# Kernel optimization log

Measured on AMD Instinct MI355X. Metric: run time of the kernel, lower is better.

The kernel has to match this reference:

```python
import jax, jax.numpy as jnp
import numpy as np

B, H, W, D = 64, 56, 56, 128
WS = 7            # window size per axis
NH = 4            # attention heads
L = 2             # transformer layers (layer 1 is shifted)
HID = 4 * D
G1, G2 = H // WS, W // WS
G, N = G1 * G2, WS * WS
SH = WS // 2      # cyclic shift


def _build_attn_mask():
    # faithful port of ShiftWindow mask construction (numpy constants)
    img = np.zeros((H, W), dtype=np.float32)
    sl = (slice(0, -WS), slice(-WS, -SH), slice(-SH, None))
    idx = 0
    for s0 in sl:
        for s1 in sl:
            img[s0, s1] = idx
            idx += 1
    win = img.reshape(G1, WS, G2, WS).transpose(0, 2, 1, 3).reshape(G, N)
    diff = win[:, None, :] - win[:, :, None]          # [G, N, N]
    return jnp.asarray(np.where(diff != 0, -100.0, 0.0).astype(np.float32))

ATTN_MASK = _build_attn_mask()


def setup_inputs() -> dict:
    key = jax.random.key(0)
    ks = jax.random.split(key, 8)
    s = 0.02
    return {
        'x': jax.random.normal(ks[0], (B, H, W, D), jnp.float32),
        'ln1_g': jnp.ones((L, D)), 'ln1_b': jnp.zeros((L, D)),
        'qkv_w': s * jax.random.normal(ks[1], (L, D, 3 * D)), 'qkv_b': jnp.zeros((L, 3 * D)),
        'proj_w': s * jax.random.normal(ks[2], (L, D, D)), 'proj_b': jnp.zeros((L, D)),
        'ln2_g': jnp.ones((L, D)), 'ln2_b': jnp.zeros((L, D)),
        'mlp_w1': s * jax.random.normal(ks[3], (L, D, HID)), 'mlp_b1': jnp.zeros((L, HID)),
        'mlp_w2': s * jax.random.normal(ks[4], (L, HID, D)), 'mlp_b2': jnp.zeros((L, D)),
        'ds_norm_g': jnp.ones((4 * D,)), 'ds_norm_b': jnp.zeros((4 * D,)),
        'ds_w': s * jax.random.normal(ks[5], (4 * D, 2 * D)),
    }


def _ln(x, g, b, eps=1e-5):
    m = jnp.mean(x, -1, keepdims=True)
    v = jnp.mean((x - m) ** 2, -1, keepdims=True)
    return (x - m) * jax.lax.rsqrt(v + eps) * g + b


def _partition(x):
    # [B, H, W, D] -> [B, G, N, D]
    x = x.reshape(B, G1, WS, G2, WS, D).transpose(0, 1, 3, 2, 4, 5)
    return x.reshape(B, G, N, D)


def _unpartition(xw):
    x = xw.reshape(B, G1, G2, WS, WS, D).transpose(0, 1, 3, 2, 4, 5)
    return x.reshape(B, H, W, D)


def _block(xw, mask, i, p):
    # pre-norm window attention
    h = _ln(xw, p['ln1_g'][i], p['ln1_b'][i])
    qkv = h @ p['qkv_w'][i] + p['qkv_b'][i]                 # [B,G,N,3D]
    q, k, v = jnp.split(qkv, 3, axis=-1)
    hd = D // NH
    q = q.reshape(B, G, N, NH, hd)
    k = k.reshape(B, G, N, NH, hd)
    v = v.reshape(B, G, N, NH, hd)
    scores = jnp.einsum('bgnhd,bgmhd->bghnm', q, k) / jnp.sqrt(jnp.float32(hd))
    if mask is not None:
        scores = scores + mask[None, :, None, :, :]         # [1,G,1,N,N]
    attn = jax.nn.softmax(scores, axis=-1)
    o = jnp.einsum('bghnm,bgmhd->bgnhd', attn, v).reshape(B, G, N, D)
    xw = xw + o @ p['proj_w'][i] + p['proj_b'][i]
    # MLP
    h = _ln(xw, p['ln2_g'][i], p['ln2_b'][i])
    h = jax.nn.gelu(h @ p['mlp_w1'][i] + p['mlp_b1'][i])
    return xw + h @ p['mlp_w2'][i] + p['mlp_b2'][i]


def reference(x, ln1_g, ln1_b, qkv_w, qkv_b, proj_w, proj_b, ln2_g, ln2_b,
              mlp_w1, mlp_b1, mlp_w2, mlp_b2, ds_norm_g, ds_norm_b, ds_w):
    p = dict(ln1_g=ln1_g, ln1_b=ln1_b, qkv_w=qkv_w, qkv_b=qkv_b,
             proj_w=proj_w, proj_b=proj_b, ln2_g=ln2_g, ln2_b=ln2_b,
             mlp_w1=mlp_w1, mlp_b1=mlp_b1, mlp_w2=mlp_w2, mlp_b2=mlp_b2)
    xw = _partition(x)
    for i in range(L):
        shift = (i % 2 == 1)
        if shift:
            xw = _partition(jnp.roll(_unpartition(xw), (-SH, -SH), axis=(1, 2)))
            xw = _block(xw, ATTN_MASK, i, p)
            xw = _partition(jnp.roll(_unpartition(xw), (SH, SH), axis=(1, 2)))
        else:
            xw = _block(xw, None, i, p)
    x = _unpartition(xw)
    # Downsample: 2x2 patch merge -> LN -> Linear(4D -> 2D) (no bias)
    x = x.reshape(B, H // 2, 2, W // 2, 2, D).transpose(0, 1, 3, 2, 4, 5)
    x = x.reshape(B, H // 2, W // 2, 4 * D)
    x = _ln(x, ds_norm_g, ds_norm_b) @ ds_w
    return x
```

## Files before the change

kernel.cpp:

```cpp
#include <hip/hip_runtime.h>
#include <hip/hip_bf16.h>


typedef short bf16x8 __attribute__((ext_vector_type(8)));
typedef float f32x4 __attribute__((ext_vector_type(4)));
typedef unsigned short u16;
typedef unsigned int u32;

#define MTOK 200704
#define DSTOK 50176

__device__ __forceinline__ u16 f2b(float f){
  u32 u = __float_as_uint(f);
  u += 0x7fffu + ((u >> 16) & 1u);
  return (u16)(u >> 16);
}
__device__ __forceinline__ float blo(u32 u){ return __uint_as_float(u << 16); }
__device__ __forceinline__ float bhi(u32 u){ return __uint_as_float(u & 0xffff0000u); }

__device__ __forceinline__ float gelu_tanh(float v){
  float u = 0.7978845608028654f * (v + 0.044715f * v * v * v);
  u = fminf(u, 10.f);
  float e = __expf(2.f * u);
  float t = (e - 1.f) / (e + 1.f);
  return 0.5f * v * (1.f + t);
}

__global__ void transpose_cvt(const float* __restrict__ src, u16* __restrict__ dst,
                              int K, int N){
  int e = blockIdx.x * 256 + threadIdx.x;
  if (e >= K * N) return;
  int k = e / N, n = e - k * N;
  dst[n * K + k] = f2b(src[e]);
}

template<int MODE>
__global__ __launch_bounds__(256) void ln_kernel(const float* __restrict__ src,
    const float* __restrict__ gw, const float* __restrict__ bw,
    u16* __restrict__ dst)
{
  int wv = threadIdx.x >> 6, lane = threadIdx.x & 63;
  int t = blockIdx.x * 4 + wv;
  long soff;
  if (MODE == 2) {
    soff = (long)t * 128;
  } else {
    int n = t % 49; int tq = t / 49; int gg = tq & 63; int b_ = tq >> 6;
    int r = n / 7, c = n - 7 * r;
    int h = (gg >> 3) * 7 + r, w = (gg & 7) * 7 + c;
    if (MODE == 1) { h += 3; if (h >= 56) h -= 56; w += 3; if (w >= 56) w -= 56; }
    soff = ((long)((b_ * 56 + h) * 56 + w)) * 128;
  }
  float2 v = *(const float2*)(src + soff + lane * 2);
  float s = v.x + v.y, s2 = v.x * v.x + v.y * v.y;
  #pragma unroll
  for (int o = 32; o; o >>= 1) { s += __shfl_xor(s, o); s2 += __shfl_xor(s2, o); }
  float mean = s * 0.0078125f;
  float var  = s2 * 0.0078125f - mean * mean;
  float rstd = rsqrtf(var + 1e-5f);
  int c0 = lane * 2;
  ushort2 o2;
  o2.x = f2b((v.x - mean) * rstd * gw[c0]   + bw[c0]);
  o2.y = f2b((v.y - mean) * rstd * gw[c0+1] + bw[c0+1]);
  *(ushort2*)(dst + (long)t * 128 + c0) = o2;
}

__global__ __launch_bounds__(256) void ds_ln_kernel(const float* __restrict__ x,
    const float* __restrict__ gw, const float* __restrict__ bw,
    u16* __restrict__ dst)
{
  int wv = threadIdx.x >> 6, lane = threadIdx.x & 63;
  int t = blockIdx.x * 4 + wv;
  int j = t % 28; int tq = t / 28; int i = tq % 28; int b_ = tq / 28;
  int e0 = lane * 8;
  int p = e0 >> 8, q = (e0 >> 7) & 1, d = e0 & 127;
  const float* src = x + ((long)((b_ * 56 + 2*i + p) * 56 + 2*j + q)) * 128 + d;
  float4 a  = *(const float4*)src;
  float4 b4 = *(const float4*)(src + 4);
  float vs[8] = {a.x, a.y, a.z, a.w, b4.x, b4.y, b4.z, b4.w};
  float s = 0.f, s2 = 0.f;
  #pragma unroll
  for (int u = 0; u < 8; u++) { s += vs[u]; s2 += vs[u] * vs[u]; }
  #pragma unroll
  for (int o = 32; o; o >>= 1) { s += __shfl_xor(s, o); s2 += __shfl_xor(s2, o); }
  float mean = s * (1.f / 512.f);
  float var  = s2 * (1.f / 512.f) - mean * mean;
  float rstd = rsqrtf(var + 1e-5f);
  u16 ov[8];
  #pragma unroll
  for (int u = 0; u < 8; u++) ov[u] = f2b((vs[u] - mean) * rstd * gw[e0+u] + bw[e0+u]);
  uint4 o4;
  o4.x = (u32)ov[0] | ((u32)ov[1] << 16);
  o4.y = (u32)ov[2] | ((u32)ov[3] << 16);
  o4.z = (u32)ov[4] | ((u32)ov[5] << 16);
  o4.w = (u32)ov[6] | ((u32)ov[7] << 16);
  *(uint4*)(dst + (long)t * 512 + e0) = o4;
}

template<int MASKED>
__global__ __launch_bounds__(256) void attn_mfma(const u16* __restrict__ qkv,
                                                 u16* __restrict__ obuf)
{
  __shared__ u16 Pls_all[4][64][72];
  const int h = threadIdx.x >> 6;
  const int lane = threadIdx.x & 63;
  const int c = lane & 15, g = lane >> 4;
  const int wi = blockIdx.x;
  const int g_ = wi & 63;
  const long t0 = (long)wi * 49;
  u16 (*Pls)[72] = Pls_all[h];

  bf16x8 qf[4], kf[4];
  #pragma unroll
  for (int mi = 0; mi < 4; mi++) {
    int r = 16*mi + c; r = r > 48 ? 48 : r;
    qf[mi] = *(const bf16x8*)(qkv + (t0 + r)*384 + h*32 + g*8);
  }
  #pragma unroll
  for (int ni = 0; ni < 4; ni++) {
    int r = 16*ni + c; r = r > 48 ? 48 : r;
    kf[ni] = *(const bf16x8*)(qkv + (t0 + r)*384 + 128 + h*32 + g*8);
  }

  f32x4 acc[4][4];
  const f32x4 zero4 = {0.f, 0.f, 0.f, 0.f};
  #pragma unroll
  for (int mi = 0; mi < 4; mi++)
    #pragma unroll
    for (int ni = 0; ni < 4; ni++)
      acc[mi][ni] = __builtin_amdgcn_mfma_f32_16x16x32_bf16(qf[mi], kf[ni], zero4, 0, 0, 0);

  bf16x8 vf[2][2];
  #pragma unroll
  for (int ni2 = 0; ni2 < 2; ni2++)
    #pragma unroll
    for (int ks = 0; ks < 2; ks++)
      #pragma unroll
      for (int jj = 0; jj < 8; jj++) {
        int k = ks*32 + 8*g + jj; k = k > 48 ? 48 : k;
        vf[ni2][ks][jj] = (short)qkv[(t0 + k)*384 + 256 + h*32 + 16*ni2 + c];
      }

  int rid_c[4];
  int g1b = 0, g2b = 0;
  if (MASKED) {
    g1b = (g_ >> 3) * 7; g2b = (g_ & 7) * 7;
    #pragma unroll
    for (int ni = 0; ni < 4; ni++) {
      int col = 16*ni + c; col = col > 48 ? 48 : col;
      int cr = col / 7, cc = col - 7*cr;
      int hh = g1b + cr, ww = g2b + cc;
      rid_c[ni] = (hh < 49 ? 0 : (hh < 53 ? 1 : 2)) * 3 + (ww < 49 ? 0 : (ww < 53 ? 1 : 2));
    }
  }

  #pragma unroll
  for (int mi = 0; mi < 4; mi++) {
    #pragma unroll
    for (int j = 0; j < 4; j++) {
      int rr = 16*mi + 4*g + j;
      int rid_r = 0;
      if (MASKED) {
        int r2 = rr > 48 ? 48 : rr;
        int rh = r2 / 7, rw = r2 - 7*rh;
        int hh = g1b + rh, ww = g2b + rw;
        rid_r = (hh < 49 ? 0 : (hh < 53 ? 1 : 2)) * 3 + (ww < 49 ? 0 : (ww < 53 ? 1 : 2));
      }
      float sv[4];
      #pragma unroll
      for (int ni = 0; ni < 4; ni++) {
        float s = acc[mi][ni][j] * 0.17677669529663687f;
        int col = 16*ni + c;
        if (col >= 49) s = -1e30f;
        else if (MASKED && rid_c[ni] != rid_r) s -= 100.f;
        sv[ni] = s;
      }
      float m4 = fmaxf(fmaxf(sv[0], sv[1]), fmaxf(sv[2], sv[3]));
      #pragma unroll
      for (int o = 1; o <= 8; o <<= 1) m4 = fmaxf(m4, __shfl_xor(m4, o));
      float p[4], sum = 0.f;
      #pragma unroll
      for (int ni = 0; ni < 4; ni++) { p[ni] = __expf(sv[ni] - m4); sum += p[ni]; }
      #pragma unroll
      for (int o = 1; o <= 8; o <<= 1) sum += __shfl_xor(sum, o);
      float rs = 1.f / sum;
      #pragma unroll
      for (int ni = 0; ni < 4; ni++)
        Pls[rr][16*ni + c] = f2b(p[ni] * rs);
    }
  }

  __syncthreads();

  f32x4 accO[4][2];
  #pragma unroll
  for (int mi = 0; mi < 4; mi++)
    #pragma unroll
    for (int ni2 = 0; ni2 < 2; ni2++) accO[mi][ni2] = zero4;
  #pragma unroll
  for (int mi = 0; mi < 4; mi++)
    #pragma unroll
    for (int ks = 0; ks < 2; ks++) {
      bf16x8 pa = *(const bf16x8*)(&Pls[16*mi + c][ks*32 + g*8]);
      #pragma unroll
      for (int ni2 = 0; ni2 < 2; ni2++)
        accO[mi][ni2] = __builtin_amdgcn_mfma_f32_16x16x32_bf16(pa, vf[ni2][ks], accO[mi][ni2], 0, 0, 0);
    }

  #pragma unroll
  for (int mi = 0; mi < 4; mi++)
    #pragma unroll
    for (int ni2 = 0; ni2 < 2; ni2++)
      #pragma unroll
      for (int j = 0; j < 4; j++) {
        int r = 16*mi + 4*g + j;
        if (r < 49)
          obuf[(t0 + r)*128 + h*32 + 16*ni2 + c] = f2b(accO[mi][ni2][j]);
      }
}

template<int K, int EPI>
__global__ __launch_bounds__(256) void gemm_kernel(
    const u16* __restrict__ A, const u16* __restrict__ Bt,
    const float* __restrict__ bias, int Ntot,
    u16* __restrict__ outb, float* __restrict__ outf,
    const float* __restrict__ resbase, int shift)
{
  __shared__ u16 As[128][72];
  __shared__ u16 Bs[128][72];
  const int tid = threadIdx.x;
  const int row0 = blockIdx.x * 128, col0 = blockIdx.y * 128;
  const int wv = tid >> 6, lane = tid & 63;
  const int m_off = (wv >> 1) * 64, n_off = (wv & 1) * 64;
  const int lr = lane & 15, lk = (lane >> 4) * 8;

  f32x4 acc[4][4];
  const f32x4 zero4 = {0.f, 0.f, 0.f, 0.f};
  #pragma unroll
  for (int a1 = 0; a1 < 4; a1++)
    #pragma unroll
    for (int a2 = 0; a2 < 4; a2++) acc[a1][a2] = zero4;

  for (int k0 = 0; k0 < K; k0 += 64) {
    __syncthreads();
    #pragma unroll
    for (int j = 0; j < 4; j++) {
      int ch = tid + 256 * j;
      int r = ch >> 3, cc = ch & 7;
      *(uint4*)(&As[r][cc*8]) = *(const uint4*)(A  + (long)(row0 + r) * K + k0 + cc*8);
      *(uint4*)(&Bs[r][cc*8]) = *(const uint4*)(Bt + (long)(col0 + r) * K + k0 + cc*8);
    }
    __syncthreads();
    #pragma unroll
    for (int kk = 0; kk < 64; kk += 32) {
      bf16x8 af[4], bfr[4];
      #pragma unroll
      for (int mi = 0; mi < 4; mi++)
        af[mi] = *(const bf16x8*)(&As[m_off + mi*16 + lr][kk + lk]);
      #pragma unroll
      for (int ni = 0; ni < 4; ni++)
        bfr[ni] = *(const bf16x8*)(&Bs[n_off + ni*16 + lr][kk + lk]);
      #pragma unroll
      for (int mi = 0; mi < 4; mi++)
        #pragma unroll
        for (int ni = 0; ni < 4; ni++)
          acc[mi][ni] = __builtin_amdgcn_mfma_f32_16x16x32_bf16(
              af[mi], bfr[ni], acc[mi][ni], 0, 0, 0);
    }
  }

  #pragma unroll
  for (int mi = 0; mi < 4; mi++) {
    #pragma unroll
    for (int j = 0; j < 4; j++) {
      int grow = row0 + m_off + mi*16 + (lane >> 4) * 4 + j;
      long obase = 0;
      if (EPI == 2) {
        int n = grow % 49; int tq = grow / 49; int gg = tq & 63; int b_ = tq >> 6;
        int r = n / 7, c = n - 7 * r;
        int hh = (gg >> 3) * 7 + r, ww = (gg & 7) * 7 + c;
        if (shift) { hh += 3; if (hh >= 56) hh -= 56; ww += 3; if (ww >= 56) ww -= 56; }
        obase = ((long)((b_ * 56 + hh) * 56 + ww)) * 128;
      }
      #pragma unroll
      for (int ni = 0; ni < 4; ni++) {
        int gcol = col0 + n_off + ni*16 + lr;
        float v = acc[mi][ni][j];
        if (EPI == 0) {
          v += bias[gcol];
          outb[(long)grow * Ntot + gcol] = f2b(v);
        } else if (EPI == 1) {
          v = gelu_tanh(v + bias[gcol]);
          outb[(long)grow * Ntot + gcol] = f2b(v);
        } else if (EPI == 2) {
          v += bias[gcol];
          outf[obase + gcol] = resbase[obase + gcol] + v;
        } else if (EPI == 3) {
          v += bias[gcol];
          outf[(long)grow * 128 + gcol] += v;
        } else {
          outf[(long)grow * Ntot + gcol] = v;
        }
      }
    }
  }
}

extern "C" void kernel_launch(void* const* d_in, const int* in_sizes, int n_in,
                              void* d_out, int out_size, void* d_ws, size_t ws_size,
                              hipStream_t stream)
{
  const float* x_in   = (const float*)d_in[0];
  const float* ln1_g  = (const float*)d_in[1];
  const float* ln1_b  = (const float*)d_in[2];
  const float* qkv_w  = (const float*)d_in[3];
  const float* qkv_b  = (const float*)d_in[4];
  const float* proj_w = (const float*)d_in[5];
  const float* proj_b = (const float*)d_in[6];
  const float* ln2_g  = (const float*)d_in[7];
  const float* ln2_b  = (const float*)d_in[8];
  const float* w1     = (const float*)d_in[9];
  const float* b1     = (const float*)d_in[10];
  const float* w2     = (const float*)d_in[11];
  const float* b2     = (const float*)d_in[12];
  const float* dsg    = (const float*)d_in[13];
  const float* dsb    = (const float*)d_in[14];
  const float* dsw    = (const float*)d_in[15];

  float* x_ws   = (float*)d_ws;
  u16* buf_h    = (u16*)(x_ws + (long)MTOK * 128);
  u16* buf_o    = buf_h;
  u16* buf_big  = buf_h + (long)MTOK * 128;
  u16* wts      = buf_big + (long)MTOK * 512;
  u16* qkv_wt   = wts;
  u16* proj_wt  = qkv_wt  + 2 * 49152;
  u16* w1t      = proj_wt + 2 * 16384;
  u16* w2t      = w1t     + 2 * 65536;
  u16* ds_wt    = w2t     + 2 * 65536;

  for (int i = 0; i < 2; i++) {
    transpose_cvt<<<(49152+255)/256, 256, 0, stream>>>(qkv_w  + i*49152, qkv_wt  + i*49152, 128, 384);
    transpose_cvt<<<(16384+255)/256, 256, 0, stream>>>(proj_w + i*16384, proj_wt + i*16384, 128, 128);
    transpose_cvt<<<(65536+255)/256, 256, 0, stream>>>(w1     + i*65536, w1t     + i*65536, 128, 512);
    transpose_cvt<<<(65536+255)/256, 256, 0, stream>>>(w2     + i*65536, w2t     + i*65536, 512, 128);
  }
  transpose_cvt<<<(131072+255)/256, 256, 0, stream>>>(dsw, ds_wt, 512, 256);

  for (int i = 0; i < 2; i++) {
    if (i == 0) ln_kernel<0><<<MTOK/4, 256, 0, stream>>>(x_in, ln1_g,       ln1_b,       buf_h);
    else        ln_kernel<1><<<MTOK/4, 256, 0, stream>>>(x_ws, ln1_g + 128, ln1_b + 128, buf_h);
    gemm_kernel<128,0><<<dim3(MTOK/128, 3), 256, 0, stream>>>(
        buf_h, qkv_wt + i*49152, qkv_b + i*384, 384, buf_big, nullptr, nullptr, 0);
    if (i == 0) attn_mfma<0><<<4096, 256, 0, stream>>>(buf_big, buf_o);
    else        attn_mfma<1><<<4096, 256, 0, stream>>>(buf_big, buf_o);
    gemm_kernel<128,2><<<dim3(MTOK/128, 1), 256, 0, stream>>>(
        buf_o, proj_wt + i*16384, proj_b + i*128, 128, nullptr, x_ws,
        (i == 0 ? x_in : (const float*)x_ws), i);
    ln_kernel<2><<<MTOK/4, 256, 0, stream>>>(x_ws, ln2_g + i*128, ln2_b + i*128, buf_h);
    gemm_kernel<128,1><<<dim3(MTOK/128, 4), 256, 0, stream>>>(
        buf_h, w1t + i*65536, b1 + i*512, 512, buf_big, nullptr, nullptr, 0);
    gemm_kernel<512,3><<<dim3(MTOK/128, 1), 256, 0, stream>>>(
        buf_big, w2t + i*65536, b2 + i*128, 128, nullptr, x_ws, x_ws, 0);
  }

  ds_ln_kernel<<<DSTOK/4, 256, 0, stream>>>(x_ws, dsg, dsb, buf_h);
  gemm_kernel<512,4><<<dim3(DSTOK/128, 2), 256, 0, stream>>>(
      buf_h, ds_wt, nullptr, 256, nullptr, (float*)d_out, nullptr, 0);
}
```

Before: 1.111 ms.

## Use direct global-to-LDS loads with XOR swizzle and LDS-staged vectorized epilogue

New measurement: 1.183 ms. 1.06x slower.

```diff
diff --git a/kernel.cpp b/kernel.cpp
--- a/kernel.cpp
+++ b/kernel.cpp
@@ -226,8 +226,11 @@
     u16* __restrict__ outb, float* __restrict__ outf,
     const float* __restrict__ resbase, int shift)
 {
-  __shared__ u16 As[128][72];
-  __shared__ u16 Bs[128][72];
+  __shared__ __align__(16) u16 sh[16384];
+  u16* Asl = sh;
+  u16* Bsl = sh + 8192;
+  float (*Cf)[128] = (float(*)[128])sh;
+
   const int tid = threadIdx.x;
   const int row0 = blockIdx.x * 128, col0 = blockIdx.y * 128;
   const int wv = tid >> 6, lane = tid & 63;
@@ -245,21 +248,30 @@
     __syncthreads();
     #pragma unroll
     for (int j = 0; j < 4; j++) {
-      int ch = tid + 256 * j;
+      int ch = tid + j * 256;
       int r = ch >> 3, cc = ch & 7;
-      *(uint4*)(&As[r][cc*8]) = *(const uint4*)(A  + (long)(row0 + r) * K + k0 + cc*8);
-      *(uint4*)(&Bs[r][cc*8]) = *(const uint4*)(Bt + (long)(col0 + r) * K + k0 + cc*8);
+      int col = k0 + ((cc * 8) ^ ((r & 7) << 3));
+      __builtin_amdgcn_global_load_lds(
+          (const __attribute__((address_space(1))) u32*)(A + (long)(row0 + r) * K + col),
+          (__attribute__((address_space(3))) u32*)(Asl + ch * 8), 16, 0, 0);
+      __builtin_amdgcn_global_load_lds(
+          (const __attribute__((address_space(1))) u32*)(Bt + (long)(col0 + r) * K + col),
+          (__attribute__((address_space(3))) u32*)(Bsl + ch * 8), 16, 0, 0);
     }
     __syncthreads();
     #pragma unroll
     for (int kk = 0; kk < 64; kk += 32) {
       bf16x8 af[4], bfr[4];
       #pragma unroll
-      for (int mi = 0; mi < 4; mi++)
-        af[mi] = *(const bf16x8*)(&As[m_off + mi*16 + lr][kk + lk]);
-      #pragma unroll
-      for (int ni = 0; ni < 4; ni++)
-        bfr[ni] = *(const bf16x8*)(&Bs[n_off + ni*16 + lr][kk + lk]);
+      for (int mi = 0; mi < 4; mi++) {
+        int R = m_off + mi*16 + lr;
+        af[mi] = *(const bf16x8*)&Asl[R*64 + ((kk + lk) ^ ((R & 7) << 3))];
+      }
+      #pragma unroll
+      for (int ni = 0; ni < 4; ni++) {
+        int R = n_off + ni*16 + lr;
+        bfr[ni] = *(const bf16x8*)&Bsl[R*64 + ((kk + lk) ^ ((R & 7) << 3))];
+      }
       #pragma unroll
       for (int mi = 0; mi < 4; mi++)
         #pragma unroll
@@ -269,38 +281,58 @@
     }
   }
 
-  #pragma unroll
-  for (int mi = 0; mi < 4; mi++) {
-    #pragma unroll
-    for (int j = 0; j < 4; j++) {
-      int grow = row0 + m_off + mi*16 + (lane >> 4) * 4 + j;
-      long obase = 0;
-      if (EPI == 2) {
+  const int g = lane >> 4;
+  #pragma unroll
+  for (int half = 0; half < 2; half++) {
+    __syncthreads();
+    if ((wv >> 1) == half) {
+      #pragma unroll
+      for (int mi = 0; mi < 4; mi++)
+        #pragma unroll
+        for (int ni = 0; ni < 4; ni++)
+          #pragma unroll
+          for (int j = 0; j < 4; j++) {
+            int lrow = mi*16 + 4*g + j;
+            int col  = n_off + ni*16 + lr;
+            Cf[lrow][col ^ ((lrow & 7) << 2)] = acc[mi][ni][j];
+          }
+    }
+    __syncthreads();
+    #pragma unroll
+    for (int jj = 0; jj < 8; jj++) {
+      int ch = tid + jj * 256;
+      int r = ch >> 5, c4 = ch & 31;
+      float4 v = *(const float4*)&Cf[r][(c4*4) ^ ((r & 7) << 2)];
+      int grow = row0 + half*64 + r;
+      int gcol = col0 + c4*4;
+      if (EPI == 0 || EPI == 1) {
+        float4 b4 = *(const float4*)&bias[gcol];
+        float v0 = v.x + b4.x, v1 = v.y + b4.y, v2 = v.z + b4.z, v3 = v.w + b4.w;
+        if (EPI == 1) { v0 = gelu_tanh(v0); v1 = gelu_tanh(v1); v2 = gelu_tanh(v2); v3 = gelu_tanh(v3); }
+        uint2 o2;
+        o2.x = (u32)f2b(v0) | ((u32)f2b(v1) << 16);
+        o2.y = (u32)f2b(v2) | ((u32)f2b(v3) << 16);
+        *(uint2*)(outb + (long)grow * Ntot + gcol) = o2;
+      } else if (EPI == 2) {
+        float4 b4 = *(const float4*)&bias[gcol];
         int n = grow % 49; int tq = grow / 49; int gg = tq & 63; int b_ = tq >> 6;
-        int r = n / 7, c = n - 7 * r;
-        int hh = (gg >> 3) * 7 + r, ww = (gg & 7) * 7 + c;
+        int rr = n / 7, cc = n - 7 * rr;
+        int hh = (gg >> 3) * 7 + rr, ww = (gg & 7) * 7 + cc;
         if (shift) { hh += 3; if (hh >= 56) hh -= 56; ww += 3; if (ww >= 56) ww -= 56; }
-        obase = ((long)((b_ * 56 + hh) * 56 + ww)) * 128;
-      }
-      #pragma unroll
-      for (int ni = 0; ni < 4; ni++) {
-        int gcol = col0 + n_off + ni*16 + lr;
-        float v = acc[mi][ni][j];
-        if (EPI == 0) {
-          v += bias[gcol];
-          outb[(long)grow * Ntot + gcol] = f2b(v);
-        } else if (EPI == 1) {
-          v = gelu_tanh(v + bias[gcol]);
-          outb[(long)grow * Ntot + gcol] = f2b(v);
-        } else if (EPI == 2) {
-          v += bias[gcol];
-          outf[obase + gcol] = resbase[obase + gcol] + v;
-        } else if (EPI == 3) {
-          v += bias[gcol];
-          outf[(long)grow * 128 + gcol] += v;
-        } else {
-          outf[(long)grow * Ntot + gcol] = v;
-        }
+        long obase = ((long)((b_ * 56 + hh) * 56 + ww)) * 128;
+        float4 res = *(const float4*)&resbase[obase + gcol];
+        float4 o;
+        o.x = res.x + v.x + b4.x; o.y = res.y + v.y + b4.y;
+        o.z = res.z + v.z + b4.z; o.w = res.w + v.w + b4.w;
+        *(float4*)&outf[obase + gcol] = o;
+      } else if (EPI == 3) {
+        float4 b4 = *(const float4*)&bias[gcol];
+        float4 cur = *(const float4*)&outf[(long)grow * 128 + gcol];
+        cur.x += v.x + b4.x; cur.y += v.y + b4.y;
+        cur.z += v.z + b4.z; cur.w += v.w + b4.w;
+        *(float4*)&outf[(long)grow * 128 + gcol] = cur;
+      } else {
+        *(float4*)&outf[(long)grow * Ntot + gcol] = v;
       }
     }
   }
```
